# Optimization experiments

Hardware: AMD Instinct MI355X
Metric: run time of the kernel (lower is better)

## Reference

```python
import jax, jax.numpy as jnp
import numpy as np

ALPHA = 0.1
DEPTH = 10
N_NODES = 100000
N_EDGES = 1600000
FEATS = 512
HIDDEN = 64
CLASSES = 64


def setup_inputs() -> dict:
    key = jax.random.key(0)
    k1, k2, k3, k4 = jax.random.split(key, 4)
    x = jax.random.normal(k1, (N_NODES, FEATS), dtype=jnp.float32)
    edges = jax.random.randint(k2, (2, N_EDGES), 0, N_NODES, dtype=jnp.int64)
    W1 = jax.random.normal(k3, (FEATS, HIDDEN), dtype=jnp.float32) * (1.0 / np.sqrt(FEATS))
    b1 = jnp.zeros((HIDDEN,), dtype=jnp.float32)
    W2 = jax.random.normal(k4, (HIDDEN, CLASSES), dtype=jnp.float32) * (1.0 / np.sqrt(HIDDEN))
    b2 = jnp.zeros((CLASSES,), dtype=jnp.float32)
    return {"x": x, "edges": edges, "W1": W1, "b1": b1, "W2": W2, "b2": b2}


def reference(x, edges, W1, b1, W2, b2):
    src, dst = edges[0], edges[1]
    # symmetric GCN normalization from edge list (in-degree over dst)
    deg = jax.ops.segment_sum(jnp.ones((N_EDGES,), jnp.float32), dst,
                              num_segments=N_NODES)
    deg = jnp.maximum(deg, 1.0)
    inv_sqrt_deg = jax.lax.rsqrt(deg)
    norm = inv_sqrt_deg[src] * inv_sqrt_deg[dst]  # [E]

    # MLP: feats -> hidden -> classes (dropout = identity in eval mode)
    h = jax.nn.relu(x @ W1 + b1)
    h = h @ W2 + b2
    h0 = h

    for _ in range(DEPTH):
        msgs = h[src] * norm[:, None]                     # [E, C] gather
        agg = jax.ops.segment_sum(msgs, dst, num_segments=N_NODES)  # scatter-add
        h = agg * (1.0 - ALPHA) + ALPHA * h0
    return h
```

## Files before the change

### kernel.cpp

```cpp
#include <hip/hip_runtime.h>
#include <hip/hip_fp16.h>

#define FEATS 512
#define HIDDEN 64
#define CLASSES 64
#define DEPTH 10
#define ALPHA 0.1f

#define NB_C 1563
#define K3_CHUNK 8192
#define K3_THREADS 512

typedef __attribute__((ext_vector_type(8))) short short8;
typedef __attribute__((ext_vector_type(4))) float f32x4;

__device__ __forceinline__ unsigned short bf16_hi(float f) {
    unsigned u = __float_as_uint(f);
    unsigned r = u + 0x7FFF + ((u >> 16) & 1);
    return (unsigned short)(r >> 16);
}
__device__ __forceinline__ float bf16_tof(unsigned short h) {
    return __uint_as_float(((unsigned)h) << 16);
}

__global__ __launch_bounds__(256) void bucket_hist_kernel(const int* __restrict__ dst,
                                                          int* __restrict__ bcnt,
                                                          int NB, int E) {
    __shared__ int h[NB_C];
    for (int j = threadIdx.x; j < NB; j += 256) h[j] = 0;
    __syncthreads();
    int i = blockIdx.x * 256 + threadIdx.x;
    int stride = gridDim.x * 256;
    for (; i < E; i += stride) atomicAdd(&h[dst[i] >> 6], 1);
    __syncthreads();
    for (int j = threadIdx.x; j < NB; j += 256) {
        int v = h[j];
        if (v) atomicAdd(&bcnt[j], v);
    }
}

__global__ __launch_bounds__(1024) void bucket_scan_kernel(const int* __restrict__ bcnt,
                                                           int* __restrict__ bptr,
                                                           int* __restrict__ gcur,
                                                           int* __restrict__ rowptr,
                                                           int NB, int N, int E) {
    __shared__ int sd[1024];
    int t = threadIdx.x;
    int i0 = 2 * t, i1 = 2 * t + 1;
    int a = (i0 < NB) ? bcnt[i0] : 0;
    int b = (i1 < NB) ? bcnt[i1] : 0;
    int s = a + b;
    sd[t] = s;
    __syncthreads();
    for (int off = 1; off < 1024; off <<= 1) {
        int v = (t >= off) ? sd[t - off] : 0;
        __syncthreads();
        sd[t] += v;
        __syncthreads();
    }
    int excl = sd[t] - s;
    if (i0 < NB) { bptr[i0] = excl;     gcur[i0] = excl; }
    if (i1 < NB) { bptr[i1] = excl + a; gcur[i1] = excl + a; }
    if (t == 0) { bptr[NB] = E; rowptr[N] = E; }
}

__global__ __launch_bounds__(K3_THREADS) void bucket_scatter_kernel(const int* __restrict__ src,
                                                                    const int* __restrict__ dst,
                                                                    int* __restrict__ gcur,
                                                                    int* __restrict__ part,
                                                                    int NB, int E) {
    __shared__ int hist[NB_C];
    __shared__ int base[NB_C];
    int cbase = blockIdx.x * K3_CHUNK;
    for (int j = threadIdx.x; j < NB; j += K3_THREADS) hist[j] = 0;
    __syncthreads();
    for (int k = 0; k < K3_CHUNK; k += K3_THREADS) {
        int i = cbase + k + threadIdx.x;
        if (i < E) atomicAdd(&hist[dst[i] >> 6], 1);
    }
    __syncthreads();
    for (int j = threadIdx.x; j < NB; j += K3_THREADS) {
        int h = hist[j];
        base[j] = (h > 0) ? atomicAdd(&gcur[j], h) : 0;
        hist[j] = 0;
    }
    __syncthreads();
    for (int k = 0; k < K3_CHUNK; k += K3_THREADS) {
        int i = cbase + k + threadIdx.x;
        if (i < E) {
            int d = dst[i];
            int j = d >> 6;
            int off = atomicAdd(&hist[j], 1);
            part[(size_t)(base[j] + off)] = (src[i] << 6) | (d & 63);
        }
    }
}

__global__ __launch_bounds__(128) void part_to_csr_kernel(const int* __restrict__ bptr,
                                                          const int* __restrict__ part,
                                                          int* __restrict__ rowptr,
                                                          float* __restrict__ inv_sqrt,
                                                          int* __restrict__ csr_src,
                                                          int N) {
    __shared__ int cnt[64];
    __shared__ int cur[64];
    int b = blockIdx.x;
    int lo = b << 6;
    int tid = threadIdx.x;
    int p0 = bptr[b], p1 = bptr[b + 1];
    if (tid < 64) cnt[tid] = 0;
    __syncthreads();
    for (int i = p0 + tid; i < p1; i += 128) {
        atomicAdd(&cnt[part[i] & 63], 1);
    }
    __syncthreads();
    if (tid < 64) {
        int v = cnt[tid];
        int incl = v;
#pragma unroll
        for (int off = 1; off < 64; off <<= 1) {
            int t = __shfl_up(incl, off);
            if (tid >= off) incl += t;
        }
        int excl = incl - v;
        if (lo + tid < N) {
            rowptr[lo + tid] = p0 + excl;
            inv_sqrt[lo + tid] = rsqrtf((float)(v < 1 ? 1 : v));
        }
        cur[tid] = excl;
    }
    __syncthreads();
    for (int i = p0 + tid; i < p1; i += 128) {
        int pe = part[i];
        int off = atomicAdd(&cur[pe & 63], 1);
        csr_src[p0 + off] = ((unsigned)pe) >> 6;
    }
}

__global__ __launch_bounds__(256) void pack_w_kernel(const float* __restrict__ W1,
                                                     const float* __restrict__ W2,
                                                     unsigned short* __restrict__ w1h,
                                                     unsigned short* __restrict__ w1l,
                                                     unsigned short* __restrict__ w2h,
                                                     unsigned short* __restrict__ w2l) {
    int id = blockIdx.x * blockDim.x + threadIdx.x;
    if (id < 4096) {
        int lane = id & 63, f = (id >> 6) & 3, ks = id >> 8;
        int col = f * 16 + (lane & 15);
        int k0 = ks * 32 + (lane >> 4) * 8;
#pragma unroll
        for (int i = 0; i < 8; ++i) {
            float v = W1[(k0 + i) * HIDDEN + col];
            unsigned short h = bf16_hi(v);
            w1h[id * 8 + i] = h;
            w1l[id * 8 + i] = bf16_hi(v - bf16_tof(h));
        }
    } else if (id < 4096 + 512) {
        int p = id - 4096;
        int lane = p & 63, f = (p >> 6) & 3, ks = p >> 8;
        int col = f * 16 + (lane & 15);
        int k0 = ks * 32 + (lane >> 4) * 8;
#pragma unroll
        for (int i = 0; i < 8; ++i) {
            float v = W2[(k0 + i) * CLASSES + col];
            unsigned short h = bf16_hi(v);
            w2h[p * 8 + i] = h;
            w2l[p * 8 + i] = bf16_hi(v - bf16_tof(h));
        }
    }
}

__global__ __launch_bounds__(256) void mlp_mfma_kernel(const float* __restrict__ x,
                                                       const unsigned short* __restrict__ w1h,
                                                       const unsigned short* __restrict__ w1l,
                                                       const float* __restrict__ b1,
                                                       const unsigned short* __restrict__ w2h,
                                                       const unsigned short* __restrict__ w2l,
                                                       const float* __restrict__ b2,
                                                       const float* __restrict__ is,
                                                       __half* __restrict__ h0h,
                                                       __half* __restrict__ u0,
                                                       int N) {
    __shared__ float hs[4][16][68];
    int wave = threadIdx.x >> 6;
    int lane = threadIdx.x & 63;
    int tile = blockIdx.x * 4 + wave;
    if (tile * 16 >= N) return;

    int row = lane & 15;
    int koff = (lane >> 4) * 8;
    const short8* w1hv = (const short8*)w1h;
    const short8* w1lv = (const short8*)w1l;
    const short8* w2hv = (const short8*)w2h;
    const short8* w2lv = (const short8*)w2l;

    f32x4 c[4] = {};
    const float* xrow = x + (size_t)(tile * 16 + row) * FEATS + koff;
#pragma unroll 4
    for (int ks = 0; ks < 16; ++ks) {
        float4 a0 = *(const float4*)(xrow + ks * 32);
        float4 a1 = *(const float4*)(xrow + ks * 32 + 4);
        float av[8] = {a0.x, a0.y, a0.z, a0.w, a1.x, a1.y, a1.z, a1.w};
        short8 ah, al;
#pragma unroll
        for (int j = 0; j < 8; ++j) {
            unsigned short h = bf16_hi(av[j]);
            ah[j] = (short)h;
            al[j] = (short)bf16_hi(av[j] - bf16_tof(h));
        }
#pragma unroll
        for (int f = 0; f < 4; ++f) {
            short8 bh = w1hv[(ks * 4 + f) * 64 + lane];
            short8 bl = w1lv[(ks * 4 + f) * 64 + lane];
            c[f] = __builtin_amdgcn_mfma_f32_16x16x32_bf16(ah, bh, c[f], 0, 0, 0);
            c[f] = __builtin_amdgcn_mfma_f32_16x16x32_bf16(ah, bl, c[f], 0, 0, 0);
            c[f] = __builtin_amdgcn_mfma_f32_16x16x32_bf16(al, bh, c[f], 0, 0, 0);
        }
    }
#pragma unroll
    for (int f = 0; f < 4; ++f) {
        float bias = b1[f * 16 + (lane & 15)];
#pragma unroll
        for (int r = 0; r < 4; ++r) {
            hs[wave][(lane >> 4) * 4 + r][f * 16 + (lane & 15)] = fmaxf(c[f][r] + bias, 0.0f);
        }
    }

    f32x4 c2[4] = {};
#pragma unroll
    for (int ks = 0; ks < 2; ++ks) {
        float4 a0 = *(const float4*)&hs[wave][row][ks * 32 + koff];
        float4 a1 = *(const float4*)&hs[wave][row][ks * 32 + koff + 4];
        float av[8] = {a0.x, a0.y, a0.z, a0.w, a1.x, a1.y, a1.z, a1.w};
        short8 ah, al;
#pragma unroll
        for (int j = 0; j < 8; ++j) {
            unsigned short h = bf16_hi(av[j]);
            ah[j] = (short)h;
            al[j] = (short)bf16_hi(av[j] - bf16_tof(h));
        }
#pragma unroll
        for (int f = 0; f < 4; ++f) {
            short8 bh = w2hv[(ks * 4 + f) * 64 + lane];
            short8 bl = w2lv[(ks * 4 + f) * 64 + lane];
            c2[f] = __builtin_amdgcn_mfma_f32_16x16x32_bf16(ah, bh, c2[f], 0, 0, 0);
            c2[f] = __builtin_amdgcn_mfma_f32_16x16x32_bf16(ah, bl, c2[f], 0, 0, 0);
            c2[f] = __builtin_amdgcn_mfma_f32_16x16x32_bf16(al, bh, c2[f], 0, 0, 0);
        }
    }
    float isv[4];
#pragma unroll
    for (int r = 0; r < 4; ++r) {
        int n = tile * 16 + (lane >> 4) * 4 + r;
        isv[r] = is[n];
    }
#pragma unroll
    for (int f = 0; f < 4; ++f) {
        float bias = b2[f * 16 + (lane & 15)];
#pragma unroll
        for (int r = 0; r < 4; ++r) {
            int n = tile * 16 + (lane >> 4) * 4 + r;
            float v = c2[f][r] + bias;
            h0h[(size_t)n * CLASSES + f * 16 + (lane & 15)] = __float2half(v);
            u0[(size_t)n * CLASSES + f * 16 + (lane & 15)] = __float2half(v * isv[r]);
        }
    }
}

__global__ __launch_bounds__(256) void prop_kernel(const int* __restrict__ rowptr,
                                                   const int* __restrict__ csr_src,
                                                   const float* __restrict__ is,
                                                   const __half* __restrict__ u_in,
                                                   const __half* __restrict__ h0h,
                                                   __half* __restrict__ u_out,
                                                   float* __restrict__ out_f32,
                                                   int N, int last) {
    int wid = (blockIdx.x * blockDim.x + threadIdx.x) >> 6;
    int lane = threadIdx.x & 63;
    if (wid >= N) return;
    int base = rowptr[wid];
    int end = rowptr[wid + 1];
    int grp = lane >> 3, sub = lane & 7;
    float acc[8] = {0.f, 0.f, 0.f, 0.f, 0.f, 0.f, 0.f, 0.f};
    for (int b = base; b < end; b += 16) {
        int e0 = b + grp;
        int e1 = e0 + 8;
        bool v0 = e0 < end;
        bool v1 = e1 < end;
        int s0 = csr_src[v0 ? e0 : base];
        int s1 = csr_src[v1 ? e1 : base];
        uint4 q0 = *(const uint4*)(u_in + ((size_t)s0 << 6) + (sub << 3));
        uint4 q1 = *(const uint4*)(u_in + ((size_t)s1 << 6) + (sub << 3));
        if (v0) {
            const __half2* hp = (const __half2*)&q0;
#pragma unroll
            for (int k = 0; k < 4; ++k) {
                float2 f2 = __half22float2(hp[k]);
                acc[2 * k] += f2.x;
                acc[2 * k + 1] += f2.y;
            }
        }
        if (v1) {
            const __half2* hp = (const __half2*)&q1;
#pragma unroll
            for (int k = 0; k < 4; ++k) {
                float2 f2 = __half22float2(hp[k]);
                acc[2 * k] += f2.x;
                acc[2 * k + 1] += f2.y;
            }
        }
    }
#pragma unroll
    for (int j = 0; j < 8; ++j) {
        acc[j] += __shfl_xor(acc[j], 8);
        acc[j] += __shfl_xor(acc[j], 16);
        acc[j] += __shfl_xor(acc[j], 32);
    }
    if (grp == 0) {
        float isd = is[wid];
        size_t rowo = ((size_t)wid << 6) + (sub << 3);
        uint4 hq = *(const uint4*)(h0h + rowo);
        const __half2* hp = (const __half2*)&hq;
        float h[8];
#pragma unroll
        for (int k = 0; k < 4; ++k) {
            float2 f2 = __half22float2(hp[k]);
            h[2 * k] = f2.x;
            h[2 * k + 1] = f2.y;
        }
        if (last) {
            float r[8];
#pragma unroll
            for (int j = 0; j < 8; ++j) r[j] = (1.0f - ALPHA) * isd * acc[j] + ALPHA * h[j];
            *(float4*)(out_f32 + rowo) = make_float4(r[0], r[1], r[2], r[3]);
            *(float4*)(out_f32 + rowo + 4) = make_float4(r[4], r[5], r[6], r[7]);
        } else {
            __half2 w[4];
#pragma unroll
            for (int k = 0; k < 4; ++k) {
                float a = ((1.0f - ALPHA) * isd * acc[2 * k] + ALPHA * h[2 * k]) * isd;
                float b = ((1.0f - ALPHA) * isd * acc[2 * k + 1] + ALPHA * h[2 * k + 1]) * isd;
                w[k] = __floats2half2_rn(a, b);
            }
            *(uint4*)(u_out + rowo) = *(uint4*)w;
        }
    }
}

extern "C" void kernel_launch(void* const* d_in, const int* in_sizes, int n_in,
                              void* d_out, int out_size, void* d_ws, size_t ws_size,
                              hipStream_t stream) {
    const float* x = (const float*)d_in[0];
    const int* edges = (const int*)d_in[1];
    const float* W1 = (const float*)d_in[2];
    const float* b1 = (const float*)d_in[3];
    const float* W2 = (const float*)d_in[4];
    const float* b2 = (const float*)d_in[5];
    float* out = (float*)d_out;

    const int N = in_sizes[0] / FEATS;
    const int E = in_sizes[1] / 2;
    const int NB = (N + 63) >> 6;
    const int* src = edges;
    const int* dst = edges + E;

    char* ws = (char*)d_ws;
    size_t off = 0;
    auto alloc = [&](size_t bytes) {
        char* p = ws + off;
        off = (off + bytes + 255) & ~(size_t)255;
        return p;
    };
    int* part = (int*)alloc((size_t)E * 4);
    int* csr_src = (int*)alloc((size_t)E * 4);
    int* bcnt = (int*)alloc((size_t)NB * 4);
    int* bptr = (int*)alloc((size_t)(NB + 1) * 4);
    int* gcur = (int*)alloc((size_t)NB * 4);
    int* rowptr = (int*)alloc((size_t)(N + 1) * 4);
    float* inv_sqrt = (float*)alloc((size_t)N * 4);
    __half* h0h = (__half*)alloc((size_t)N * CLASSES * 2);
    __half* uA = (__half*)alloc((size_t)N * CLASSES * 2);
    __half* uB = (__half*)alloc((size_t)N * CLASSES * 2);
    unsigned short* w1h = (unsigned short*)alloc(4096 * 8 * 2);
    unsigned short* w1l = (unsigned short*)alloc(4096 * 8 * 2);
    unsigned short* w2h = (unsigned short*)alloc(512 * 8 * 2);
    unsigned short* w2l = (unsigned short*)alloc(512 * 8 * 2);
    (void)ws_size;

    hipMemsetAsync(bcnt, 0, (size_t)NB * 4, stream);
    bucket_hist_kernel<<<128, 256, 0, stream>>>(dst, bcnt, NB, E);
    bucket_scan_kernel<<<1, 1024, 0, stream>>>(bcnt, bptr, gcur, rowptr, NB, N, E);
    int k3_blocks = (E + K3_CHUNK - 1) / K3_CHUNK;
    bucket_scatter_kernel<<<k3_blocks, K3_THREADS, 0, stream>>>(src, dst, gcur, part, NB, E);
    part_to_csr_kernel<<<NB, 128, 0, stream>>>(bptr, part, rowptr, inv_sqrt, csr_src, N);

    pack_w_kernel<<<18, 256, 0, stream>>>(W1, W2, w1h, w1l, w2h, w2l);
    int tiles = (N + 15) / 16;
    mlp_mfma_kernel<<<(tiles + 3) / 4, 256, 0, stream>>>(x, w1h, w1l, b1, w2h, w2l, b2,
                                                         inv_sqrt, h0h, uA, N);

    int blocks = (N * 64 + 255) / 256;
    for (int d = 0; d < DEPTH; ++d) {
        const __half* uin = (d & 1) ? uB : uA;
        __half* uout = (d & 1) ? uA : uB;
        int last = (d == DEPTH - 1);
        prop_kernel<<<blocks, 256, 0, stream>>>(rowptr, csr_src, inv_sqrt, uin, h0h,
                                                uout, out, N, last);
    }
}
```

Before: 607.0 us.

## Split propagation into four 16-column feature planes for cache locality

The MLP now writes h0 and u0 as four planar 16-column slices instead of row-major 64-column rows. Propagation runs all ten depth iterations separately for each slice, with two nodes per wave and a 32-byte gather per edge. The aim is to shrink the randomly gathered working set so it stays resident in L2. The cost is four times as many launches and four times as many CSR index reads, plus less work per wave.

Measured after the change: 1.063 ms. +75.2%, slower.

```diff
diff --git a/kernel.cpp b/kernel.cpp
--- a/kernel.cpp
+++ b/kernel.cpp
@@ -178,7 +178,7 @@
                                                        const unsigned short* __restrict__ w2l,
                                                        const float* __restrict__ b2,
                                                        const float* __restrict__ is,
-                                                       __half* __restrict__ h0h,
+                                                       __half* __restrict__ h0q,
                                                        __half* __restrict__ u0,
                                                        int N) {
     __shared__ float hs[4][16][68];
@@ -261,38 +261,36 @@
         for (int r = 0; r < 4; ++r) {
             int n = tile * 16 + (lane >> 4) * 4 + r;
             float v = c2[f][r] + bias;
-            h0h[(size_t)n * CLASSES + f * 16 + (lane & 15)] = __float2half(v);
-            u0[(size_t)n * CLASSES + f * 16 + (lane & 15)] = __float2half(v * isv[r]);
-        }
-    }
-}
-
-__global__ __launch_bounds__(256) void prop_kernel(const int* __restrict__ rowptr,
-                                                   const int* __restrict__ csr_src,
-                                                   const float* __restrict__ is,
-                                                   const __half* __restrict__ u_in,
-                                                   const __half* __restrict__ h0h,
-                                                   __half* __restrict__ u_out,
-                                                   float* __restrict__ out_f32,
-                                                   int N, int last) {
-    int wid = (blockIdx.x * blockDim.x + threadIdx.x) >> 6;
+            size_t po = ((size_t)f * N + n) * 16 + (lane & 15);
+            h0q[po] = __float2half(v);
+            u0[po] = __float2half(v * isv[r]);
+        }
+    }
+}
+
+__global__ __launch_bounds__(256) void propq_kernel(const int* __restrict__ rowptr,
+                                                    const int* __restrict__ csr_src,
+                                                    const float* __restrict__ is,
+                                                    const __half* __restrict__ u_in,
+                                                    const __half* __restrict__ h0q,
+                                                    __half* __restrict__ u_out,
+                                                    float* __restrict__ out_f32,
+                                                    int N, int q, int last) {
+    int wpair = (blockIdx.x * 256 + threadIdx.x) >> 6;
     int lane = threadIdx.x & 63;
-    if (wid >= N) return;
-    int base = rowptr[wid];
-    int end = rowptr[wid + 1];
-    int grp = lane >> 3, sub = lane & 7;
+    int half = lane >> 5;
+    int hl = lane & 31;
+    int node = wpair * 2 + half;
+    if (node >= N) return;
+    int grp = hl >> 1, sub = hl & 1;
+    int base = rowptr[node], end = rowptr[node + 1];
     float acc[8] = {0.f, 0.f, 0.f, 0.f, 0.f, 0.f, 0.f, 0.f};
     for (int b = base; b < end; b += 16) {
-        int e0 = b + grp;
-        int e1 = e0 + 8;
-        bool v0 = e0 < end;
-        bool v1 = e1 < end;
-        int s0 = csr_src[v0 ? e0 : base];
-        int s1 = csr_src[v1 ? e1 : base];
-        uint4 q0 = *(const uint4*)(u_in + ((size_t)s0 << 6) + (sub << 3));
-        uint4 q1 = *(const uint4*)(u_in + ((size_t)s1 << 6) + (sub << 3));
-        if (v0) {
-            const __half2* hp = (const __half2*)&q0;
+        int e = b + grp;
+        if (e < end) {
+            int s = csr_src[e];
+            uint4 qv = *(const uint4*)(u_in + ((size_t)s << 4) + (sub << 3));
+            const __half2* hp = (const __half2*)&qv;
 #pragma unroll
             for (int k = 0; k < 4; ++k) {
                 float2 f2 = __half22float2(hp[k]);
@@ -300,26 +298,18 @@
                 acc[2 * k + 1] += f2.y;
             }
         }
-        if (v1) {
-            const __half2* hp = (const __half2*)&q1;
-#pragma unroll
-            for (int k = 0; k < 4; ++k) {
-                float2 f2 = __half22float2(hp[k]);
-                acc[2 * k] += f2.x;
-                acc[2 * k + 1] += f2.y;
-            }
-        }
     }
 #pragma unroll
     for (int j = 0; j < 8; ++j) {
+        acc[j] += __shfl_xor(acc[j], 2);
+        acc[j] += __shfl_xor(acc[j], 4);
         acc[j] += __shfl_xor(acc[j], 8);
         acc[j] += __shfl_xor(acc[j], 16);
-        acc[j] += __shfl_xor(acc[j], 32);
     }
     if (grp == 0) {
-        float isd = is[wid];
-        size_t rowo = ((size_t)wid << 6) + (sub << 3);
-        uint4 hq = *(const uint4*)(h0h + rowo);
+        float isd = is[node];
+        size_t rowo = ((size_t)node << 4) + (sub << 3);
+        uint4 hq = *(const uint4*)(h0q + rowo);
         const __half2* hp = (const __half2*)&hq;
         float h[8];
 #pragma unroll
@@ -332,8 +322,9 @@
             float r[8];
 #pragma unroll
             for (int j = 0; j < 8; ++j) r[j] = (1.0f - ALPHA) * isd * acc[j] + ALPHA * h[j];
-            *(float4*)(out_f32 + rowo) = make_float4(r[0], r[1], r[2], r[3]);
-            *(float4*)(out_f32 + rowo + 4) = make_float4(r[4], r[5], r[6], r[7]);
+            float4* op = (float4*)(out_f32 + (size_t)node * 64 + q * 16 + sub * 8);
+            op[0] = make_float4(r[0], r[1], r[2], r[3]);
+            op[1] = make_float4(r[4], r[5], r[6], r[7]);
         } else {
             __half2 w[4];
 #pragma unroll
@@ -378,7 +369,7 @@
     int* gcur = (int*)alloc((size_t)NB * 4);
     int* rowptr = (int*)alloc((size_t)(N + 1) * 4);
     float* inv_sqrt = (float*)alloc((size_t)N * 4);
-    __half* h0h = (__half*)alloc((size_t)N * CLASSES * 2);
+    __half* h0q = (__half*)alloc((size_t)N * CLASSES * 2);
     __half* uA = (__half*)alloc((size_t)N * CLASSES * 2);
     __half* uB = (__half*)alloc((size_t)N * CLASSES * 2);
     unsigned short* w1h = (unsigned short*)alloc(4096 * 8 * 2);
@@ -397,14 +388,17 @@
     pack_w_kernel<<<18, 256, 0, stream>>>(W1, W2, w1h, w1l, w2h, w2l);
     int tiles = (N + 15) / 16;
     mlp_mfma_kernel<<<(tiles + 3) / 4, 256, 0, stream>>>(x, w1h, w1l, b1, w2h, w2l, b2,
-                                                         inv_sqrt, h0h, uA, N);
-
-    int blocks = (N * 64 + 255) / 256;
-    for (int d = 0; d < DEPTH; ++d) {
-        const __half* uin = (d & 1) ? uB : uA;
-        __half* uout = (d & 1) ? uA : uB;
-        int last = (d == DEPTH - 1);
-        prop_kernel<<<blocks, 256, 0, stream>>>(rowptr, csr_src, inv_sqrt, uin, h0h,
-                                                uout, out, N, last);
-    }
-}
+                                                         inv_sqrt, h0q, uA, N);
+
+    int blocks = ((N + 1) / 2 * 64 + 255) / 256;
+    for (int q = 0; q < 4; ++q) {
+        size_t plane = (size_t)q * N * 16;
+        for (int d = 0; d < DEPTH; ++d) {
+            const __half* uin = ((d & 1) ? uB : uA) + plane;
+            __half* uout = ((d & 1) ? uA : uB) + plane;
+            int last = (d == DEPTH - 1);
+            propq_kernel<<<blocks, 256, 0, stream>>>(rowptr, csr_src, inv_sqrt, uin,
+                                                     h0q + plane, uout, out, N, q, last);
+        }
+    }
+}
```
